# Optimization experiments

Hardware: AMD Instinct MI355X
Metric: run time of the kernel (lower is better)

Reference implementation:

```python
import jax, jax.numpy as jnp
import numpy as np

B, HW, C, H = 4, 2048, 768, 8
HD = C // H  # 96


def _rotate_half_interleaved(t):
    # t: [..., HD]; pairs (t1, t2) at even/odd positions -> (-t2, t1) interleaved
    t1 = t[..., ::2]
    t2 = t[..., 1::2]
    return jnp.stack([-t2, t1], axis=-1).reshape(t.shape)


def setup_inputs() -> dict:
    key = jax.random.key(0)
    kx, kq, kp, kb = jax.random.split(key, 4)
    x = jax.random.normal(kx, (B, HW, C), dtype=jnp.float32)
    # standard interleaved RoPE tables: freq repeated pairwise along head_dim
    inv_freq = 1.0 / (10000.0 ** (np.arange(0, HD, 2, dtype=np.float32) / HD))  # [HD/2]
    angles = np.arange(HW, dtype=np.float32)[:, None] * inv_freq[None, :]        # [HW, HD/2]
    angles = np.repeat(angles, 2, axis=-1)                                        # [HW, HD]
    cos = jnp.asarray(np.cos(angles), dtype=jnp.float32)
    sin = jnp.asarray(np.sin(angles), dtype=jnp.float32)
    Wqkv = jax.random.normal(kq, (3 * C, C), dtype=jnp.float32) * (C ** -0.5)
    Wproj = jax.random.normal(kp, (C, C), dtype=jnp.float32) * (C ** -0.5)
    bproj = jnp.zeros((C,), dtype=jnp.float32)
    return {"x": x, "cos": cos, "sin": sin, "Wqkv": Wqkv, "Wproj": Wproj, "bproj": bproj}


def reference(x, cos, sin, Wqkv, Wproj, bproj):
    Bv, hw, Cv = x.shape
    scale = HD ** -0.5
    qkv = x @ Wqkv.T                                  # [B, hw, 3C]
    qkv = qkv.reshape(Bv, hw, 3, H, HD).transpose(2, 0, 3, 1, 4)  # [3, B, H, hw, HD]
    q, k, v = qkv[0], qkv[1], qkv[2]
    # RoPE: broadcast cos/sin [hw, HD] over [B, H, hw, HD]
    cosb = cos[None, None, :, :]
    sinb = sin[None, None, :, :]
    q = q * cosb + _rotate_half_interleaved(q) * sinb
    k = k * cosb + _rotate_half_interleaved(k) * sinb
    attn = jnp.einsum('bhqd,bhkd->bhqk', q, k) * scale
    attn = jax.nn.softmax(attn, axis=-1)
    out = jnp.einsum('bhqk,bhkd->bhqd', attn, v)      # [B, H, hw, HD]
    out = out.transpose(0, 2, 1, 3).reshape(Bv, hw, Cv)
    return out @ Wproj.T + bproj
```

## Files before the change

kernel.cpp:

```cpp
#include <hip/hip_runtime.h>
#include <hip/hip_bf16.h>
#include <math.h>

#define Bc  4
#define HWc 2048
#define Cc  768
#define Hc  8
#define HDc 96

typedef short bf16x8 __attribute__((ext_vector_type(8)));
typedef float f32x4  __attribute__((ext_vector_type(4)));

static __device__ __forceinline__ unsigned short f2bf(float x) {
    __hip_bfloat16 h = __float2bfloat16(x);
    return *reinterpret_cast<unsigned short*>(&h);
}

#define GLOBAL_AS(p) ((const __attribute__((address_space(1))) void*)(p))
#define LDS_AS(p)    ((__attribute__((address_space(3))) void*)(p))

__global__ __launch_bounds__(256) void cast_bf16(
    const float* __restrict__ src, unsigned short* __restrict__ dst, int n4)
{
    int i = blockIdx.x * 256 + threadIdx.x;
    if (i < n4) {
        float4 v = ((const float4*)src)[i];
        ushort4 p;
        p.x = f2bf(v.x); p.y = f2bf(v.y); p.z = f2bf(v.z); p.w = f2bf(v.w);
        ((ushort4*)dst)[i] = p;
    }
}

__global__ __launch_bounds__(256) void qkv_mfma_T(
    const unsigned short* __restrict__ Wb, const unsigned short* __restrict__ xb,
    const float* __restrict__ cs, const float* __restrict__ sn,
    unsigned short* __restrict__ qo, unsigned short* __restrict__ ko,
    unsigned short* __restrict__ vt)
{
    __shared__ unsigned short Al[128 * 32];
    __shared__ unsigned short Bl[128 * 32];
    const int tid  = threadIdx.x;
    const int lane = tid & 63;
    const int w    = tid >> 6;
    const int c    = lane & 15, qd = lane >> 4;
    const int wm   = w & 1, wn = w >> 1;
    const int m0   = blockIdx.y << 7;
    const int n0   = blockIdx.x << 7;

    const int srow = (w << 5) + (lane >> 2);
    const int sseg = (lane & 3) << 3;
    const unsigned short* Ag = Wb + (size_t)(m0 + srow) * Cc + sseg;
    const unsigned short* Bg = xb + (size_t)(n0 + srow) * Cc + sseg;
    unsigned short* Adst = &Al[(w << 5) * 32];
    unsigned short* Bdst = &Bl[(w << 5) * 32];

    f32x4 acc[4][4];
    #pragma unroll
    for (int i = 0; i < 4; i++)
        #pragma unroll
        for (int j = 0; j < 4; j++) acc[i][j] = (f32x4)0.f;

    for (int k0 = 0; k0 < Cc; k0 += 32) {
        __syncthreads();
        __builtin_amdgcn_global_load_lds(GLOBAL_AS(Ag + k0),            LDS_AS(Adst),            16, 0, 0);
        __builtin_amdgcn_global_load_lds(GLOBAL_AS(Ag + 16 * Cc + k0),  LDS_AS(Adst + 16 * 32),  16, 0, 0);
        __builtin_amdgcn_global_load_lds(GLOBAL_AS(Bg + k0),            LDS_AS(Bdst),            16, 0, 0);
        __builtin_amdgcn_global_load_lds(GLOBAL_AS(Bg + 16 * Cc + k0),  LDS_AS(Bdst + 16 * 32),  16, 0, 0);
        __syncthreads();

        bf16x8 af[4], bfr[4];
        #pragma unroll
        for (int mt = 0; mt < 4; mt++)
            af[mt] = *(const bf16x8*)&Al[((wm << 6) + mt * 16 + c) * 32 + qd * 8];
        #pragma unroll
        for (int nt = 0; nt < 4; nt++)
            bfr[nt] = *(const bf16x8*)&Bl[((wn << 6) + nt * 16 + c) * 32 + qd * 8];
        #pragma unroll
        for (int mt = 0; mt < 4; mt++)
            #pragma unroll
            for (int nt = 0; nt < 4; nt++)
                acc[mt][nt] = __builtin_amdgcn_mfma_f32_16x16x32_bf16(
                    af[mt], bfr[nt], acc[mt][nt], 0, 0, 0);
    }

    const int which = m0 / Cc;
    const int m0l = m0 - which * Cc;
    const float qs = 0.10206207261596577f;

    if (which == 2) {
        #pragma unroll
        for (int mt = 0; mt < 4; mt++) {
            const int c0 = m0l + (wm << 6) + mt * 16 + (qd << 2);
            const int h = c0 / HDc, d = c0 % HDc;
            #pragma unroll
            for (int nt = 0; nt < 4; nt++) {
                const int t = n0 + (wn << 6) + nt * 16 + c;
                const int b = t >> 11, tt = t & (HWc - 1);
                const size_t base = ((size_t)((b * Hc + h) * HDc + d)) * HWc + tt;
                #pragma unroll
                for (int r = 0; r < 4; r++)
                    vt[base + (size_t)r * HWc] = f2bf(acc[mt][nt][r]);
            }
        }
    } else {
        unsigned short* dst = which ? ko : qo;
        const float sc = which ? 1.0f : qs;
        #pragma unroll
        for (int mt = 0; mt < 4; mt++) {
            const int c0 = m0l + (wm << 6) + mt * 16 + (qd << 2);
            const int h = c0 / HDc, d = c0 % HDc;
            #pragma unroll
            for (int nt = 0; nt < 4; nt++) {
                const int t = n0 + (wn << 6) + nt * 16 + c;
                const int b = t >> 11, tt = t & (HWc - 1);
                const float4 c4 = *(const float4*)&cs[tt * HDc + d];
                const float4 s4 = *(const float4*)&sn[tt * HDc + d];
                float o0 = (acc[mt][nt][0] * c4.x - acc[mt][nt][1] * s4.x) * sc;
                float o1 = (acc[mt][nt][1] * c4.y + acc[mt][nt][0] * s4.y) * sc;
                float o2 = (acc[mt][nt][2] * c4.z - acc[mt][nt][3] * s4.z) * sc;
                float o3 = (acc[mt][nt][3] * c4.w + acc[mt][nt][2] * s4.w) * sc;
                ushort4 pk;
                pk.x = f2bf(o0); pk.y = f2bf(o1); pk.z = f2bf(o2); pk.w = f2bf(o3);
                *(ushort4*)&dst[((size_t)(b * Hc + h) * HWc + tt) * HDc + d] = pk;
            }
        }
    }
}

__global__ __launch_bounds__(256, 4) void attn_flash(
    const unsigned short* __restrict__ qg, const unsigned short* __restrict__ kg,
    const unsigned short* __restrict__ vtg, unsigned short* __restrict__ ob)
{
    __shared__ unsigned short Ks[64][104];
    __shared__ unsigned short Vt[96][72];
    __shared__ unsigned short Pt[4][16][72];

    const int tid  = threadIdx.x;
    const int lane = tid & 63;
    const int w    = tid >> 6;
    const int c    = lane & 15;
    const int qd   = lane >> 4;
    const int bh   = blockIdx.y;
    const int b    = bh >> 3, h = bh & 7;
    const int q0   = blockIdx.x << 6;

    const unsigned short* kb  = kg  + (size_t)bh * HWc * HDc;
    const unsigned short* vtb = vtg + (size_t)bh * HDc * HWc;

    bf16x8 qt[3];
    {
        const unsigned short* qr = qg + ((size_t)bh * HWc + q0 + w * 16 + c) * HDc + qd * 8;
        #pragma unroll
        for (int ks = 0; ks < 3; ks++)
            qt[ks] = *(const bf16x8*)(qr + ks * 32);
    }

    f32x4 oacc[6];
    #pragma unroll
    for (int mt = 0; mt < 6; mt++) oacc[mt] = (f32x4)0.f;
    float lsum = 0.f;

    for (int ck = 0; ck < 32; ck++) {
        __syncthreads();
        {
            const unsigned short* kc = kb + (size_t)(ck << 6) * HDc;
            #pragma unroll
            for (int it = 0; it < 3; it++) {
                int idx = tid + (it << 8);
                int row = idx / 12, seg = idx - row * 12;
                uint4 val = *(const uint4*)(kc + row * HDc + seg * 8);
                *(uint4*)&Ks[row][seg * 8] = val;
            }
            const unsigned short* vc = vtb + (ck << 6);
            #pragma unroll
            for (int it = 0; it < 3; it++) {
                int idx = tid + (it << 8);
                int row = idx >> 3, seg = idx & 7;
                uint4 val = *(const uint4*)(vc + (size_t)row * HWc + seg * 8);
                *(uint4*)&Vt[row][seg * 8] = val;
            }
        }
        __syncthreads();

        f32x4 sacc[4];
        #pragma unroll
        for (int mt = 0; mt < 4; mt++) sacc[mt] = (f32x4)0.f;
        #pragma unroll
        for (int mt = 0; mt < 4; mt++)
            #pragma unroll
            for (int ks = 0; ks < 3; ks++) {
                bf16x8 af = *(const bf16x8*)&Ks[mt * 16 + c][ks * 32 + qd * 8];
                sacc[mt] = __builtin_amdgcn_mfma_f32_16x16x32_bf16(
                    af, qt[ks], sacc[mt], 0, 0, 0);
            }

        float rs = 0.f;
        #pragma unroll
        for (int mt = 0; mt < 4; mt++)
            #pragma unroll
            for (int r = 0; r < 4; r++) {
                float p = __expf(sacc[mt][r]);
                sacc[mt][r] = p;
                rs += p;
            }
        rs += __shfl_xor(rs, 16);
        rs += __shfl_xor(rs, 32);
        lsum += rs;

        #pragma unroll
        for (int mt = 0; mt < 4; mt++) {
            __hip_bfloat162 p01 = __float22bfloat162_rn(float2{sacc[mt][0], sacc[mt][1]});
            __hip_bfloat162 p23 = __float22bfloat162_rn(float2{sacc[mt][2], sacc[mt][3]});
            uint2 pk;
            pk.x = *reinterpret_cast<unsigned int*>(&p01);
            pk.y = *reinterpret_cast<unsigned int*>(&p23);
            *(uint2*)&Pt[w][c][mt * 16 + qd * 4] = pk;
        }
        bf16x8 pf[2];
        #pragma unroll
        for (int ks = 0; ks < 2; ks++)
            pf[ks] = *(const bf16x8*)&Pt[w][c][ks * 32 + qd * 8];

        #pragma unroll
        for (int mt = 0; mt < 6; mt++)
            #pragma unroll
            for (int ks = 0; ks < 2; ks++) {
                bf16x8 vf = *(const bf16x8*)&Vt[mt * 16 + c][ks * 32 + qd * 8];
                oacc[mt] = __builtin_amdgcn_mfma_f32_16x16x32_bf16(
                    vf, pf[ks], oacc[mt], 0, 0, 0);
            }
    }

    const float linv = 1.0f / lsum;
    unsigned short* orow = ob + ((size_t)(b * HWc + q0 + w * 16 + c)) * Cc + h * HDc;
    #pragma unroll
    for (int mt = 0; mt < 6; mt++) {
        f32x4 val = oacc[mt] * linv;
        ushort4 pk;
        pk.x = f2bf(val[0]); pk.y = f2bf(val[1]);
        pk.z = f2bf(val[2]); pk.w = f2bf(val[3]);
        *(ushort4*)&orow[mt * 16 + qd * 4] = pk;
    }
}

__global__ __launch_bounds__(256) void proj_mfma_T(
    const unsigned short* __restrict__ Wb, const unsigned short* __restrict__ Ab,
    const float* __restrict__ bias, float* __restrict__ out)
{
    __shared__ unsigned short Al[128 * 32];
    __shared__ unsigned short Bl[128 * 32];
    const int tid  = threadIdx.x;
    const int lane = tid & 63;
    const int w    = tid >> 6;
    const int c    = lane & 15, qd = lane >> 4;
    const int wm   = w & 1, wn = w >> 1;
    const int m0   = blockIdx.y << 7;
    const int n0   = blockIdx.x << 7;

    const int srow = (w << 5) + (lane >> 2);
    const int sseg = (lane & 3) << 3;
    const unsigned short* Ag = Wb + (size_t)(m0 + srow) * Cc + sseg;
    const unsigned short* Bg = Ab + (size_t)(n0 + srow) * Cc + sseg;
    unsigned short* Adst = &Al[(w << 5) * 32];
    unsigned short* Bdst = &Bl[(w << 5) * 32];

    f32x4 acc[4][4];
    #pragma unroll
    for (int i = 0; i < 4; i++)
        #pragma unroll
        for (int j = 0; j < 4; j++) acc[i][j] = (f32x4)0.f;

    for (int k0 = 0; k0 < Cc; k0 += 32) {
        __syncthreads();
        __builtin_amdgcn_global_load_lds(GLOBAL_AS(Ag + k0),           LDS_AS(Adst),           16, 0, 0);
        __builtin_amdgcn_global_load_lds(GLOBAL_AS(Ag + 16 * Cc + k0), LDS_AS(Adst + 16 * 32), 16, 0, 0);
        __builtin_amdgcn_global_load_lds(GLOBAL_AS(Bg + k0),           LDS_AS(Bdst),           16, 0, 0);
        __builtin_amdgcn_global_load_lds(GLOBAL_AS(Bg + 16 * Cc + k0), LDS_AS(Bdst + 16 * 32), 16, 0, 0);
        __syncthreads();

        bf16x8 af[4], bfr[4];
        #pragma unroll
        for (int mt = 0; mt < 4; mt++)
            af[mt] = *(const bf16x8*)&Al[((wm << 6) + mt * 16 + c) * 32 + qd * 8];
        #pragma unroll
        for (int nt = 0; nt < 4; nt++)
            bfr[nt] = *(const bf16x8*)&Bl[((wn << 6) + nt * 16 + c) * 32 + qd * 8];
        #pragma unroll
        for (int mt = 0; mt < 4; mt++)
            #pragma unroll
            for (int nt = 0; nt < 4; nt++)
                acc[mt][nt] = __builtin_amdgcn_mfma_f32_16x16x32_bf16(
                    af[mt], bfr[nt], acc[mt][nt], 0, 0, 0);
    }

    #pragma unroll
    for (int mt = 0; mt < 4; mt++) {
        const int f = m0 + (wm << 6) + mt * 16 + (qd << 2);
        const float4 b4 = *(const float4*)&bias[f];
        #pragma unroll
        for (int nt = 0; nt < 4; nt++) {
            const int t = n0 + (wn << 6) + nt * 16 + c;
            float4 val;
            val.x = acc[mt][nt][0] + b4.x;
            val.y = acc[mt][nt][1] + b4.y;
            val.z = acc[mt][nt][2] + b4.z;
            val.w = acc[mt][nt][3] + b4.w;
            *(float4*)&out[(size_t)t * Cc + f] = val;
        }
    }
}

extern "C" void kernel_launch(void* const* d_in, const int* in_sizes, int n_in,
                              void* d_out, int out_size, void* d_ws, size_t ws_size,
                              hipStream_t stream) {
    const float* x     = (const float*)d_in[0];
    const float* cs    = (const float*)d_in[1];
    const float* sn    = (const float*)d_in[2];
    const float* Wqkv  = (const float*)d_in[3];
    const float* Wproj = (const float*)d_in[4];
    const float* bproj = (const float*)d_in[5];
    float* out = (float*)d_out;

    const size_t per = (size_t)Bc * Hc * HWc * HDc;
    const size_t nx  = per;
    const size_t nwq = (size_t)3 * Cc * Cc;
    const size_t nwp = (size_t)Cc * Cc;

    unsigned short* xb  = (unsigned short*)d_ws;
    unsigned short* Wqb = xb + nx;
    unsigned short* Wpb = Wqb + nwq;
    unsigned short* q   = Wpb + nwp;
    unsigned short* k   = q + per;
    unsigned short* vt  = k + per;
    unsigned short* ob  = vt + per;

    cast_bf16<<<dim3((int)(nx / 4 + 255) / 256), 256, 0, stream>>>(x, xb, (int)(nx / 4));
    cast_bf16<<<dim3((int)(nwq / 4 + 255) / 256), 256, 0, stream>>>(Wqkv, Wqb, (int)(nwq / 4));
    cast_bf16<<<dim3((int)(nwp / 4 + 255) / 256), 256, 0, stream>>>(Wproj, Wpb, (int)(nwp / 4));

    qkv_mfma_T<<<dim3(64, 18), 256, 0, stream>>>(Wqb, xb, cs, sn, q, k, vt);
    attn_flash<<<dim3(32, 32), 256, 0, stream>>>(q, k, vt, ob);
    proj_mfma_T<<<dim3(64, 6), 256, 0, stream>>>(Wpb, ob, bproj, out);
}
```

Baseline: 289.5 us.

## Merge cast kernels, stage Q/K epilogue through LDS, swap attention grid order

```diff
diff --git a/kernel.cpp b/kernel.cpp
--- a/kernel.cpp
+++ b/kernel.cpp
@@ -19,16 +19,22 @@
 #define GLOBAL_AS(p) ((const __attribute__((address_space(1))) void*)(p))
 #define LDS_AS(p)    ((__attribute__((address_space(3))) void*)(p))
 
-__global__ __launch_bounds__(256) void cast_bf16(
-    const float* __restrict__ src, unsigned short* __restrict__ dst, int n4)
+__global__ __launch_bounds__(256) void cast_all(
+    const float* __restrict__ x, const float* __restrict__ Wq,
+    const float* __restrict__ Wp, unsigned short* __restrict__ xb,
+    unsigned short* __restrict__ Wqb, unsigned short* __restrict__ Wpb,
+    int nx4, int nwq4, int nwp4)
 {
     int i = blockIdx.x * 256 + threadIdx.x;
-    if (i < n4) {
-        float4 v = ((const float4*)src)[i];
-        ushort4 p;
-        p.x = f2bf(v.x); p.y = f2bf(v.y); p.z = f2bf(v.z); p.w = f2bf(v.w);
-        ((ushort4*)dst)[i] = p;
-    }
+    const float* src; unsigned short* dst; int j = i;
+    if (i < nx4) { src = x; dst = xb; }
+    else if ((j = i - nx4) < nwq4) { src = Wq; dst = Wqb; }
+    else if ((j = i - nx4 - nwq4) < nwp4) { src = Wp; dst = Wpb; }
+    else return;
+    float4 v = ((const float4*)src)[j];
+    ushort4 p;
+    p.x = f2bf(v.x); p.y = f2bf(v.y); p.z = f2bf(v.z); p.w = f2bf(v.w);
+    ((ushort4*)dst)[j] = p;
 }
 
 __global__ __launch_bounds__(256) void qkv_mfma_T(
@@ -39,6 +45,7 @@
 {
     __shared__ unsigned short Al[128 * 32];
     __shared__ unsigned short Bl[128 * 32];
+    __shared__ unsigned short Tt[64][132];
     const int tid  = threadIdx.x;
     const int lane = tid & 63;
     const int w    = tid >> 6;
@@ -105,23 +112,41 @@
     } else {
         unsigned short* dst = which ? ko : qo;
         const float sc = which ? 1.0f : qs;
-        #pragma unroll
-        for (int mt = 0; mt < 4; mt++) {
-            const int c0 = m0l + (wm << 6) + mt * 16 + (qd << 2);
-            const int h = c0 / HDc, d = c0 % HDc;
-            #pragma unroll
-            for (int nt = 0; nt < 4; nt++) {
-                const int t = n0 + (wn << 6) + nt * 16 + c;
-                const int b = t >> 11, tt = t & (HWc - 1);
-                const float4 c4 = *(const float4*)&cs[tt * HDc + d];
-                const float4 s4 = *(const float4*)&sn[tt * HDc + d];
-                float o0 = (acc[mt][nt][0] * c4.x - acc[mt][nt][1] * s4.x) * sc;
-                float o1 = (acc[mt][nt][1] * c4.y + acc[mt][nt][0] * s4.y) * sc;
-                float o2 = (acc[mt][nt][2] * c4.z - acc[mt][nt][3] * s4.z) * sc;
-                float o3 = (acc[mt][nt][3] * c4.w + acc[mt][nt][2] * s4.w) * sc;
-                ushort4 pk;
-                pk.x = f2bf(o0); pk.y = f2bf(o1); pk.z = f2bf(o2); pk.w = f2bf(o3);
-                *(ushort4*)&dst[((size_t)(b * Hc + h) * HWc + tt) * HDc + d] = pk;
+        for (int tk = 0; tk < 2; tk++) {
+            __syncthreads();
+            if (wn == tk) {
+                #pragma unroll
+                for (int mt = 0; mt < 4; mt++) {
+                    const int c0 = m0l + (wm << 6) + mt * 16 + (qd << 2);
+                    const int d = c0 % HDc;
+                    #pragma unroll
+                    for (int nt = 0; nt < 4; nt++) {
+                        const int t = n0 + (wn << 6) + nt * 16 + c;
+                        const int tt = t & (HWc - 1);
+                        const float4 c4 = *(const float4*)&cs[tt * HDc + d];
+                        const float4 s4 = *(const float4*)&sn[tt * HDc + d];
+                        float o0 = (acc[mt][nt][0] * c4.x - acc[mt][nt][1] * s4.x) * sc;
+                        float o1 = (acc[mt][nt][1] * c4.y + acc[mt][nt][0] * s4.y) * sc;
+                        float o2 = (acc[mt][nt][2] * c4.z - acc[mt][nt][3] * s4.z) * sc;
+                        float o3 = (acc[mt][nt][3] * c4.w + acc[mt][nt][2] * s4.w) * sc;
+                        ushort4 pk;
+                        pk.x = f2bf(o0); pk.y = f2bf(o1);
+                        pk.z = f2bf(o2); pk.w = f2bf(o3);
+                        *(ushort4*)&Tt[nt * 16 + c][(wm << 6) + mt * 16 + (qd << 2)] = pk;
+                    }
+                }
+            }
+            __syncthreads();
+            #pragma unroll
+            for (int it = 0; it < 8; it++) {
+                int s = tid + (it << 8);
+                int row = s >> 5, fseg = (s & 31) << 2;
+                int fg = m0l + fseg;
+                int h = fg / HDc, d = fg % HDc;
+                int token = n0 + tk * 64 + row;
+                int b = token >> 11, tt = token & (HWc - 1);
+                *(ushort4*)&dst[((size_t)(b * Hc + h) * HWc + tt) * HDc + d] =
+                    *(ushort4*)&Tt[row][fseg];
             }
         }
     }
@@ -140,9 +165,9 @@
     const int w    = tid >> 6;
     const int c    = lane & 15;
     const int qd   = lane >> 4;
-    const int bh   = blockIdx.y;
+    const int bh   = blockIdx.x;
     const int b    = bh >> 3, h = bh & 7;
-    const int q0   = blockIdx.x << 6;
+    const int q0   = blockIdx.y << 6;
 
     const unsigned short* kb  = kg  + (size_t)bh * HWc * HDc;
     const unsigned short* vtb = vtg + (size_t)bh * HDc * HWc;
@@ -334,9 +359,10 @@
     unsigned short* vt  = k + per;
     unsigned short* ob  = vt + per;
 
-    cast_bf16<<<dim3((int)(nx / 4 + 255) / 256), 256, 0, stream>>>(x, xb, (int)(nx / 4));
-    cast_bf16<<<dim3((int)(nwq / 4 + 255) / 256), 256, 0, stream>>>(Wqkv, Wqb, (int)(nwq / 4));
-    cast_bf16<<<dim3((int)(nwp / 4 + 255) / 256), 256, 0, stream>>>(Wproj, Wpb, (int)(nwp / 4));
+    const int nx4 = (int)(nx / 4), nwq4 = (int)(nwq / 4), nwp4 = (int)(nwp / 4);
+    const int ntot = nx4 + nwq4 + nwp4;
+    cast_all<<<dim3((ntot + 255) / 256), 256, 0, stream>>>(
+        x, Wqkv, Wproj, xb, Wqb, Wpb, nx4, nwq4, nwp4);
 
     qkv_mfma_T<<<dim3(64, 18), 256, 0, stream>>>(Wqb, xb, cs, sn, q, k, vt);
     attn_flash<<<dim3(32, 32), 256, 0, stream>>>(q, k, vt, ob);
```

After: 286.2 us. Within noise of the previous version (-1.1%).
